# Optimization experiments

Measured on AMD Instinct MI355X. Metric: run time of the kernel, lower is better.

## Reference

```python
import jax, jax.numpy as jnp
import numpy as np

NFPS = 10

def setup_inputs() -> dict:
    key = jax.random.key(0)
    k1, k2, k3, k4 = jax.random.split(key, 4)
    B, D_IN, H, D_OUT = 131072, 2 * NFPS * 3, 256, NFPS * 3 * 12
    x = jax.random.normal(k1, (B, D_IN), dtype=jnp.float32)
    centres = jax.random.normal(k2, (H, D_IN), dtype=jnp.float32)
    sigmas = jax.random.uniform(k3, (H,), dtype=jnp.float32)
    W2 = jax.random.normal(k4, (D_OUT, H), dtype=jnp.float32) * (1.0 / np.sqrt(H))
    return {"x": x, "centres": centres, "sigmas": sigmas, "W2": W2}

def reference(x, centres, sigmas, W2):
    # RBF layer: distances = ||x - c|| * sigma; gaussian: exp(-distances^2)
    x2 = jnp.sum(x * x, axis=-1, keepdims=True)            # [B,1]
    c2 = jnp.sum(centres * centres, axis=-1)               # [H]
    xc = jnp.einsum('bd,hd->bh', x, centres)               # [B,H]
    d2 = jnp.maximum(x2 + c2[None, :] - 2.0 * xc, 0.0)     # squared distance, clamp fp noise
    phi = jnp.exp(-(sigmas[None, :] ** 2) * d2)            # [B,H]
    out = jnp.einsum('bh,oh->bo', phi, W2)                 # [B, nFPs*3*12]
    B = x.shape[0]
    out = out.reshape(B, NFPS, 12, 3).transpose(0, 1, 3, 2).reshape(B, 3 * NFPS, 12)
    return out
```

## Files before the change

kernel.cpp:

```cpp
#include <hip/hip_runtime.h>

#define THREADS 512
#define DIN 60
#define HN 256
#define DOUT 360

typedef __attribute__((ext_vector_type(8))) short short8;
typedef __attribute__((ext_vector_type(16))) float f32x16;
typedef __attribute__((ext_vector_type(4))) float f32x4;
typedef __attribute__((ext_vector_type(4))) unsigned int u32x4;

#define WS_CBF   0
#define WS_W2    32768

__device__ __forceinline__ short bf16_bits(float f) {
    union { float f; unsigned u; } v; v.f = f;
    unsigned r = (v.u + 0x7FFFu + ((v.u >> 16) & 1u)) >> 16;
    return (short)(unsigned short)r;
}

__device__ __forceinline__ unsigned pk_bf16(float a, float b) {
    unsigned r;
    asm("v_cvt_pk_bf16_f32 %0, %1, %2" : "=v"(r) : "v"(a), "v"(b));
    return r;
}

__device__ __forceinline__ void gload16(const void* g, void* lds) {
    __builtin_amdgcn_global_load_lds(
        (const __attribute__((address_space(1))) unsigned int*)(uintptr_t)g,
        (__attribute__((address_space(3))) unsigned int*)(unsigned int)(uintptr_t)lds,
        16, 0, 0);
}

__global__ void prep(const float* __restrict__ centres, const float* __restrict__ sigmas,
                     const float* __restrict__ W2, short* __restrict__ ws)
{
    int t = blockIdx.x * 256 + threadIdx.x;
    if (t < 12288) {
        int row = t >> 5, pc = t & 31;
        int c = pc ^ (row & 31);
        short8 v = {0,0,0,0,0,0,0,0};
        if (row < DOUT) {
            int rr = row / 12, jj = row % 12;
            int fcl = rr / 3, kk = rr % 3;
            int o = fcl * 36 + jj * 3 + kk;
            const float* src = W2 + o * HN + c * 8;
            #pragma unroll
            for (int i = 0; i < 8; ++i) v[i] = bf16_bits(src[i]);
        }
        *(short8*)(ws + (WS_W2 / 2) + t * 8) = v;
    } else if (t < 14336) {
        int j = t - 12288;
        int row = j >> 3, p = j & 7;
        int c = p ^ (row & 7);
        const float* cr = centres + row * DIN;
        float sg = sigmas[row];
        union { unsigned u; float f; } nq;
        nq.u = ((unsigned)(unsigned short)bf16_bits(2.f * sg * sg * 1.44269504088896340736f)) << 16;
        const float nsq = nq.f;
        short8 v = {0,0,0,0,0,0,0,0};
        if (c < 7) {
            #pragma unroll
            for (int i = 0; i < 8; ++i) {
                int k = c * 8 + i;
                if (k < DIN) v[i] = bf16_bits(nsq * cr[k]);
            }
        } else {
            #pragma unroll
            for (int i = 0; i < 4; ++i) v[i] = bf16_bits(nsq * cr[56 + i]);
            float c2 = 0.f;
            #pragma unroll
            for (int d = 0; d < DIN; ++d) c2 = fmaf(cr[d], cr[d], c2);
            float T = -0.5f * nsq * c2;
            union { unsigned u; float f; } th;
            th.u = ((unsigned)(unsigned short)bf16_bits(T)) << 16;
            v[4] = bf16_bits(th.f);
            v[5] = bf16_bits(T - th.f);
            v[6] = bf16_bits(-0.5f * nsq);
            v[7] = v[6];
        }
        *(short8*)(ws + (WS_CBF / 2) + j * 8) = v;
    }
}

__device__ __forceinline__ void load_xtile(const float* __restrict__ x, int row0,
                                           int l31, int hi, short8 xb[4]) {
    const float* xr = x + (size_t)(row0 + l31) * DIN;
    f32x4 xa[4][2];
    #pragma unroll
    for (int kt = 0; kt < 4; ++kt) {
        int k0 = kt * 16 + hi * 8;
        xa[kt][0] = *(const f32x4*)(xr + k0);
        xa[kt][1] = (k0 + 4 < DIN) ? *(const f32x4*)(xr + k0 + 4) : (f32x4){0.f,0.f,0.f,0.f};
    }
    float p2 = 0.f;
    #pragma unroll
    for (int kt = 0; kt < 4; ++kt)
        #pragma unroll
        for (int h = 0; h < 2; ++h)
            #pragma unroll
            for (int i = 0; i < 4; ++i) p2 = fmaf(xa[kt][h][i], xa[kt][h][i], p2);
    float x2v = p2 + __shfl_xor(p2, 32);
    union { unsigned u; float f; } hb; hb.u = pk_bf16(x2v, 0.f) << 16;
    float x2lo = x2v - hb.f;
    #pragma unroll
    for (int kt = 0; kt < 4; ++kt) {
        union { u32x4 u; short8 s; } a;
        a.u[0] = pk_bf16(xa[kt][0][0], xa[kt][0][1]);
        a.u[1] = pk_bf16(xa[kt][0][2], xa[kt][0][3]);
        a.u[2] = pk_bf16(xa[kt][1][0], xa[kt][1][1]);
        a.u[3] = pk_bf16(xa[kt][1][2], xa[kt][1][3]);
        if (kt == 3) {
            a.u[2] = hi ? 0x3F803F80u : a.u[2];
            a.u[3] = hi ? pk_bf16(hb.f, x2lo) : a.u[3];
        }
        xb[kt] = a.s;
    }
}

__global__ __attribute__((amdgpu_flat_work_group_size(THREADS, THREADS),
                          amdgpu_waves_per_eu(2, 2)))
void rbf_main(const float* __restrict__ x, const short* __restrict__ ws,
              float* __restrict__ out)
{
    __shared__ short8 w2h[6144];
    __shared__ short8 cbf[2048];

    const int tid  = threadIdx.x;
    const int w    = tid >> 6;
    const int lane = tid & 63;
    const int l31  = lane & 31;
    const int hi   = lane >> 5;
    const int bid  = blockIdx.x;
    const int f     = (bid >> 3) & 1;
    const int sbase = (bid & 7) | ((bid >> 4) << 3);

    #pragma unroll
    for (int i = 0; i < 12; ++i)
        gload16(ws + (WS_W2 / 2) + ((size_t)f * 6144 + i * THREADS + tid) * 8,
                (char*)w2h + (i * THREADS + tid) * 16);
    #pragma unroll
    for (int i = 0; i < 4; ++i)
        gload16(ws + (WS_CBF / 2) + (i * THREADS + tid) * 8, (char*)cbf + (i * THREADS + tid) * 16);

    short8 xb[4];
    load_xtile(x, sbase * 1024 + w * 32, l31, hi, xb);

    __syncthreads();

    for (int it = 0; it < 4; ++it) {
        const int rb = sbase * 1024 + it * 256 + w * 32;

        f32x16 acc2[6];
        #pragma unroll
        for (int nt = 0; nt < 6; ++nt) acc2[nt] = (f32x16){};

        #pragma unroll
        for (int nt1 = 0; nt1 < 8; ++nt1) {
            f32x16 a1 = (f32x16){};
            const int row = nt1 * 32 + l31;
            __builtin_amdgcn_s_setprio(1);
            #pragma unroll
            for (int kt = 0; kt < 4; ++kt) {
                short8 cf = cbf[row * 8 + ((kt * 2 + hi) ^ (row & 7))];
                a1 = __builtin_amdgcn_mfma_f32_32x32x16_bf16(cf, xb[kt], a1, 0, 0, 0);
            }
            __builtin_amdgcn_s_setprio(0);

            unsigned pwl[4][2];
            #pragma unroll
            for (int q = 0; q < 4; ++q) {
                float ph[4];
                #pragma unroll
                for (int j = 0; j < 4; ++j)
                    ph[j] = exp2f(fminf(a1[4 * q + j], 0.f));
                pwl[q][0] = pk_bf16(ph[0], ph[1]);
                pwl[q][1] = pk_bf16(ph[2], ph[3]);
            }

            #pragma unroll
            for (int m = 0; m < 2; ++m) {
                unsigned d0 = pwl[2 * m][0], s0 = pwl[2 * m + 1][0];
                unsigned d1 = pwl[2 * m][1], s1 = pwl[2 * m + 1][1];
                asm("v_permlane32_swap_b32 %0, %1" : "+v"(d0), "+v"(s0));
                asm("v_permlane32_swap_b32 %0, %1" : "+v"(d1), "+v"(s1));
                union { u32x4 u; short8 s; } bfr;
                bfr.u[0] = d0; bfr.u[1] = d1; bfr.u[2] = s0; bfr.u[3] = s1;
                const int ktg = nt1 * 2 + m;

                __builtin_amdgcn_s_setprio(1);
                #pragma unroll
                for (int nt = 0; nt < 6; ++nt) {
                    int lrow = nt * 32 + l31;
                    short8 wf = w2h[lrow * 32 + ((ktg * 2 + hi) ^ l31)];
                    acc2[nt] = __builtin_amdgcn_mfma_f32_32x32x16_bf16(wf, bfr.s, acc2[nt], 0, 0, 0);
                }
                __builtin_amdgcn_s_setprio(0);
            }
        }

        if (it < 3)
            load_xtile(x, rb + 256, l31, hi, xb);

        {
            float* op = out + (size_t)(rb + l31) * DOUT;
            #pragma unroll
            for (int nt = 0; nt < 6; ++nt) {
                #pragma unroll
                for (int q = 0; q < 4; ++q) {
                    int col = f * 192 + nt * 32 + q * 8 + hi * 4;
                    if (col < DOUT) {
                        f32x4 v;
                        v[0] = acc2[nt][4 * q + 0]; v[1] = acc2[nt][4 * q + 1];
                        v[2] = acc2[nt][4 * q + 2]; v[3] = acc2[nt][4 * q + 3];
                        *(f32x4*)(op + col) = v;
                    }
                }
            }
        }
    }
}

extern "C" void kernel_launch(void* const* d_in, const int* in_sizes, int n_in,
                              void* d_out, int out_size, void* d_ws, size_t ws_size,
                              hipStream_t stream) {
    const float* x       = (const float*)d_in[0];
    const float* centres = (const float*)d_in[1];
    const float* sigmas  = (const float*)d_in[2];
    const float* W2      = (const float*)d_in[3];
    float* out = (float*)d_out;
    short* ws  = (short*)d_ws;
    prep<<<dim3(56), dim3(256), 0, stream>>>(centres, sigmas, W2, ws);
    rbf_main<<<dim3(256), dim3(THREADS), 0, stream>>>(x, ws, out);
}
```

Baseline: 62.88 us.

## Stream W2 fragments from global into double-buffered registers instead of LDS

W2 is re-laid out in the workspace in k-chunk-major order, so each lane can load its MFMA B-fragments directly from global/L2 into registers. A two-stage register double buffer prefetches the next k-step's twelve fragments during the current step. This drops the 96KB LDS staging of W2 and its LDS reads, which frees LDS and cuts LDS bandwidth. The next x tile load moves after the output stores. In exchange it adds many more VGPRs (24 short8 buffers) under a 2-waves-per-EU bound, and every block repeatedly fetches W2 from cache.

Result: slower. 198.5 us (+215.7%).

```diff
diff --git a/kernel.cpp b/kernel.cpp
--- a/kernel.cpp
+++ b/kernel.cpp
@@ -37,14 +37,13 @@
 {
     int t = blockIdx.x * 256 + threadIdx.x;
     if (t < 12288) {
-        int row = t >> 5, pc = t & 31;
-        int c = pc ^ (row & 31);
+        int kc = t / 384, row = t % 384;
         short8 v = {0,0,0,0,0,0,0,0};
         if (row < DOUT) {
             int rr = row / 12, jj = row % 12;
             int fcl = rr / 3, kk = rr % 3;
             int o = fcl * 36 + jj * 3 + kk;
-            const float* src = W2 + o * HN + c * 8;
+            const float* src = W2 + o * HN + kc * 8;
             #pragma unroll
             for (int i = 0; i < 8; ++i) v[i] = bf16_bits(src[i]);
         }
@@ -123,7 +122,6 @@
 void rbf_main(const float* __restrict__ x, const short* __restrict__ ws,
               float* __restrict__ out)
 {
-    __shared__ short8 w2h[6144];
     __shared__ short8 cbf[2048];
 
     const int tid  = threadIdx.x;
@@ -136,17 +134,22 @@
     const int sbase = (bid & 7) | ((bid >> 4) << 3);
 
     #pragma unroll
-    for (int i = 0; i < 12; ++i)
-        gload16(ws + (WS_W2 / 2) + ((size_t)f * 6144 + i * THREADS + tid) * 8,
-                (char*)w2h + (i * THREADS + tid) * 16);
-    #pragma unroll
     for (int i = 0; i < 4; ++i)
         gload16(ws + (WS_CBF / 2) + (i * THREADS + tid) * 8, (char*)cbf + (i * THREADS + tid) * 16);
 
+    const short8* const wfb = (const short8*)(ws + (WS_W2 / 2))
+                              + (size_t)(hi * 384 + f * 192 + l31);
+
     short8 xb[4];
     load_xtile(x, sbase * 1024 + w * 32, l31, hi, xb);
 
     __syncthreads();
+
+    short8 buf[2][12];
+    const short8* pA = wfb;
+    const short8* pB = wfb + 768;
+    #pragma unroll
+    for (int j = 0; j < 6; ++j) { buf[0][j] = pA[j * 32]; buf[0][6 + j] = pB[j * 32]; }
 
     for (int it = 0; it < 4; ++it) {
         const int rb = sbase * 1024 + it * 256 + w * 32;
@@ -157,6 +160,16 @@
 
         #pragma unroll
         for (int nt1 = 0; nt1 < 8; ++nt1) {
+            const int cur = nt1 & 1;
+
+            if (nt1 < 7) { pA += 1536; pB += 1536; }
+            else         { pA = wfb;   pB = wfb + 768; }
+            #pragma unroll
+            for (int j = 0; j < 6; ++j) {
+                buf[cur ^ 1][j]     = pA[j * 32];
+                buf[cur ^ 1][6 + j] = pB[j * 32];
+            }
+
             f32x16 a1 = (f32x16){};
             const int row = nt1 * 32 + l31;
             __builtin_amdgcn_s_setprio(1);
@@ -186,21 +199,15 @@
                 asm("v_permlane32_swap_b32 %0, %1" : "+v"(d1), "+v"(s1));
                 union { u32x4 u; short8 s; } bfr;
                 bfr.u[0] = d0; bfr.u[1] = d1; bfr.u[2] = s0; bfr.u[3] = s1;
-                const int ktg = nt1 * 2 + m;
 
                 __builtin_amdgcn_s_setprio(1);
                 #pragma unroll
-                for (int nt = 0; nt < 6; ++nt) {
-                    int lrow = nt * 32 + l31;
-                    short8 wf = w2h[lrow * 32 + ((ktg * 2 + hi) ^ l31)];
-                    acc2[nt] = __builtin_amdgcn_mfma_f32_32x32x16_bf16(wf, bfr.s, acc2[nt], 0, 0, 0);
-                }
+                for (int nt = 0; nt < 6; ++nt)
+                    acc2[nt] = __builtin_amdgcn_mfma_f32_32x32x16_bf16(
+                        buf[cur][m * 6 + nt], bfr.s, acc2[nt], 0, 0, 0);
                 __builtin_amdgcn_s_setprio(0);
             }
         }
-
-        if (it < 3)
-            load_xtile(x, rb + 256, l31, hi, xb);
 
         {
             float* op = out + (size_t)(rb + l31) * DOUT;
@@ -218,6 +225,9 @@
                 }
             }
         }
+
+        if (it < 3)
+            load_xtile(x, rb + 256, l31, hi, xb);
     }
 }
 
```
